# Performance work log

Measured on AMD Instinct MI355X. Metric: run time of the kernel, lower is better.

## Reference

```python
import jax, jax.numpy as jnp
import numpy as np

D_MODEL = 1024
N_HEADS = 16
HEAD_DIM = D_MODEL // N_HEADS


def setup_inputs() -> dict:
    key = jax.random.key(0)
    ks = jax.random.split(key, 5)
    B, T = 2, 2048
    x = jax.random.normal(ks[0], (B, T, D_MODEL), dtype=jnp.float32)
    s_in = 1.0 / np.sqrt(D_MODEL)
    W_qkv = jax.random.normal(ks[1], (D_MODEL, 3 * D_MODEL), dtype=jnp.float32) * s_in
    b_qkv = jnp.zeros((3 * D_MODEL,), dtype=jnp.float32)
    W_out = jax.random.normal(ks[2], (D_MODEL, D_MODEL), dtype=jnp.float32) * s_in
    b_out = jnp.zeros((D_MODEL,), dtype=jnp.float32)
    gamma = jnp.ones((D_MODEL,), dtype=jnp.float32)
    beta = jnp.zeros((D_MODEL,), dtype=jnp.float32)
    return {"x": x, "W_qkv": W_qkv, "b_qkv": b_qkv, "W_out": W_out,
            "b_out": b_out, "gamma": gamma, "beta": beta}


def _layernorm(x, gamma, beta, eps=1e-5):
    mu = jnp.mean(x, axis=-1, keepdims=True)
    var = jnp.var(x, axis=-1, keepdims=True)
    return (x - mu) * jax.lax.rsqrt(var + eps) * gamma + beta


def reference(x, W_qkv, b_qkv, W_out, b_out, gamma, beta):
    B, T, D = x.shape
    residual = x
    h = _layernorm(x, gamma, beta)
    qkv = h @ W_qkv + b_qkv                      # [B, T, 3D]
    qkv = qkv.reshape(B, T, 3, N_HEADS, HEAD_DIM)
    q = jnp.transpose(qkv[:, :, 0], (0, 2, 1, 3))  # [B, H, T, hd]
    k = jnp.transpose(qkv[:, :, 1], (0, 2, 1, 3))
    v = jnp.transpose(qkv[:, :, 2], (0, 2, 1, 3))
    scale = 1.0 / np.sqrt(HEAD_DIM)
    attn = jnp.einsum("bhqd,bhkd->bhqk", q, k) * scale
    attn = jax.nn.softmax(attn, axis=-1)
    out = jnp.einsum("bhqk,bhkd->bhqd", attn, v)   # [B, H, T, hd]
    out = jnp.transpose(out, (0, 2, 1, 3)).reshape(B, T, D)
    out = out @ W_out + b_out
    return residual + out
```

## Files before the change

kernel.cpp:

```cpp
#include <hip/hip_runtime.h>
#include <hip/hip_bf16.h>


#define DINL static __device__ __forceinline__

typedef __attribute__((ext_vector_type(8))) short bf16x8;
typedef __attribute__((ext_vector_type(4))) float f32x4;

DINL float fast_exp2(float x) { return __builtin_amdgcn_exp2f(x); }

DINL unsigned short f2bf(float f) {
  __hip_bfloat16 h = __float2bfloat16(f);
  unsigned short u;
  __builtin_memcpy(&u, &h, 2);
  return u;
}

DINL unsigned int bfbits(float f) {
  unsigned int u;
  __builtin_memcpy(&u, &f, 4);
  return (u + 0x8000u) >> 16;
}

DINL void gload_lds16(const void* g, void* l) {
  __builtin_amdgcn_global_load_lds((__attribute__((address_space(1))) void*)g,
                                   (__attribute__((address_space(3))) void*)l,
                                   16, 0, 0);
}

__global__ __launch_bounds__(256)
void ln_kernel(const float* __restrict__ x, const float* __restrict__ gamma,
               const float* __restrict__ beta, unsigned short* __restrict__ h) {
  __shared__ float red[8];
  int row = blockIdx.x;
  int t = threadIdx.x;
  float4 v = reinterpret_cast<const float4*>(x + (size_t)row * 1024)[t];
  float s  = v.x + v.y + v.z + v.w;
  float sq = v.x*v.x + v.y*v.y + v.z*v.z + v.w*v.w;
#pragma unroll
  for (int off = 1; off < 64; off <<= 1) {
    s  += __shfl_xor(s, off);
    sq += __shfl_xor(sq, off);
  }
  int wid = t >> 6;
  if ((t & 63) == 0) { red[wid] = s; red[4 + wid] = sq; }
  __syncthreads();
  s  = red[0] + red[1] + red[2] + red[3];
  sq = red[4] + red[5] + red[6] + red[7];
  float mu   = s * (1.0f / 1024.0f);
  float var  = sq * (1.0f / 1024.0f) - mu * mu;
  float rstd = rsqrtf(var + 1e-5f);
  float4 g = reinterpret_cast<const float4*>(gamma)[t];
  float4 b = reinterpret_cast<const float4*>(beta)[t];
  ushort4 o;
  o.x = f2bf((v.x - mu) * rstd * g.x + b.x);
  o.y = f2bf((v.y - mu) * rstd * g.y + b.y);
  o.z = f2bf((v.z - mu) * rstd * g.z + b.z);
  o.w = f2bf((v.w - mu) * rstd * g.w + b.w);
  reinterpret_cast<ushort4*>(h + (size_t)row * 1024)[t] = o;
}

__global__ __launch_bounds__(256)
void transpose_cast_kernel(const float* __restrict__ src, unsigned short* __restrict__ dst,
                           int R, int C) {
  __shared__ float tile[32][33];
  int tx = threadIdx.x & 31, ty = threadIdx.x >> 5;
  int c0 = blockIdx.x * 32, r0 = blockIdx.y * 32;
#pragma unroll
  for (int i = 0; i < 4; i++)
    tile[ty + i * 8][tx] = src[(size_t)(r0 + ty + i * 8) * C + c0 + tx];
  __syncthreads();
#pragma unroll
  for (int i = 0; i < 4; i++) {
    int r = ty + i * 8;
    dst[(size_t)(c0 + r) * R + r0 + tx] = f2bf(tile[tx][r]);
  }
}

template <int MODE>
__global__ __launch_bounds__(256)
void gemm128(const unsigned short* __restrict__ A,
             const unsigned short* __restrict__ Bt,
             int K,
             const float* __restrict__ bias,
             unsigned short* __restrict__ qdst, unsigned short* __restrict__ kdst,
             unsigned short* __restrict__ vTdst,
             const float* __restrict__ xres, float* __restrict__ out) {
  __shared__ unsigned short As[8192];
  __shared__ unsigned short Bs[8192];
  int tid = threadIdx.x, wid = tid >> 6, lane = tid & 63;
  int l15 = lane & 15, l4 = lane >> 4;
  int brow = blockIdx.y * 128, bcol = blockIdx.x * 128;
  int wr = wid >> 1, wc = wid & 1;
  f32x4 acc[4][4] = {};

  for (int kt = 0; kt < K; kt += 64) {
    __syncthreads();
#pragma unroll
    for (int r = 0; r < 4; r++) {
      int c  = wid * 256 + r * 64;
      int cl = c + lane;
      int kb = cl >> 7, row = cl & 127;
      gload_lds16(A  + (size_t)(brow + row) * K + kt + kb * 8, As + c * 8);
      gload_lds16(Bt + (size_t)(bcol + row) * K + kt + kb * 8, Bs + c * 8);
    }
    __syncthreads();
#pragma unroll
    for (int ks = 0; ks < 2; ks++) {
      int kb = ks * 4 + l4;
      bf16x8 af[4], bfr[4];
#pragma unroll
      for (int m = 0; m < 4; m++)
        af[m] = *reinterpret_cast<const bf16x8*>(As + (kb * 128 + wr * 64 + m * 16 + l15) * 8);
#pragma unroll
      for (int n = 0; n < 4; n++)
        bfr[n] = *reinterpret_cast<const bf16x8*>(Bs + (kb * 128 + wc * 64 + n * 16 + l15) * 8);
#pragma unroll
      for (int m = 0; m < 4; m++)
#pragma unroll
        for (int n = 0; n < 4; n++)
          acc[m][n] = __builtin_amdgcn_mfma_f32_16x16x32_bf16(af[m], bfr[n], acc[m][n], 0, 0, 0);
    }
  }

  if (MODE == 0) {
    int sec = bcol >> 10;
    int secbase = sec << 10;
#pragma unroll
    for (int m = 0; m < 4; m++) {
      int row0 = brow + wr * 64 + m * 16 + l4 * 4;
      int b = row0 >> 11, t0 = row0 & 2047;
#pragma unroll
      for (int n = 0; n < 4; n++) {
        int col = (bcol & 1023) + wc * 64 + n * 16 + l15;
        float bv = bias[secbase + col];
        int hh = col >> 6, d = col & 63;
        if (sec == 2) {
          ushort4 pk;
          pk.x = f2bf(acc[m][n][0] + bv);
          pk.y = f2bf(acc[m][n][1] + bv);
          pk.z = f2bf(acc[m][n][2] + bv);
          pk.w = f2bf(acc[m][n][3] + bv);
          *reinterpret_cast<ushort4*>(vTdst + ((size_t)(b * 16 + hh) * 64 + d) * 2048 + t0) = pk;
        } else {
          unsigned short* dst = (sec == 0) ? qdst : kdst;
          float sc = (sec == 0) ? 0.125f * 1.44269504088896f : 1.0f;
#pragma unroll
          for (int j = 0; j < 4; j++)
            dst[((size_t)(b * 16 + hh) * 2048 + t0 + j) * 64 + d] = f2bf((acc[m][n][j] + bv) * sc);
        }
      }
    }
  } else {
#pragma unroll
    for (int m = 0; m < 4; m++) {
      int row0 = brow + wr * 64 + m * 16 + l4 * 4;
#pragma unroll
      for (int n = 0; n < 4; n++) {
        int col = bcol + wc * 64 + n * 16 + l15;
        float bv = bias[col];
#pragma unroll
        for (int j = 0; j < 4; j++) {
          size_t idx = (size_t)(row0 + j) * 1024 + col;
          out[idx] = acc[m][n][j] + bv + xres[idx];
        }
      }
    }
  }
}

__global__ __launch_bounds__(256, 2)
void attn_kernel(const unsigned short* __restrict__ q,
                 const unsigned short* __restrict__ kk,
                 const unsigned short* __restrict__ vT,
                 unsigned short* __restrict__ o) {
  const int T = 2048;
  __shared__ unsigned short Ks[2][8192];
  __shared__ unsigned short Ps[4][2048];
  int tid = threadIdx.x, wid = tid >> 6, lane = tid & 63;
  int l15 = lane & 15, l4 = lane >> 4;
  int swz = (l15 & 7) << 3;

  int lin = blockIdx.x;
  int rl  = (lin & 7) * 64 + (lin >> 3);
  int bx = rl & 15, bh = rl >> 4;
  int q0 = bx * 128 + wid * 32;

  const unsigned short* qh = q  + (size_t)bh * T * 64;
  const unsigned short* kh = kk + (size_t)bh * T * 64;
  const unsigned short* vh = vT + (size_t)bh * 64 * T;

  bf16x8 qf[2][2];
#pragma unroll
  for (int m = 0; m < 2; m++)
#pragma unroll
    for (int ks = 0; ks < 2; ks++)
      qf[m][ks] = *reinterpret_cast<const bf16x8*>(
          qh + (size_t)(q0 + m * 16 + l15) * 64 + ks * 32 + l4 * 8);

  f32x4 accO[2][4] = {};
  float mst[2] = {-1e30f, -1e30f}, lst[2] = {0.0f, 0.0f};

#define STAGE128(buf, kv0)                                                     \
  {                                                                            \
    _Pragma("unroll") for (int r = 0; r < 4; r++) {                            \
      int c  = (wid * 4 + r) * 64;                                             \
      int cl = c + lane;                                                       \
      int key = cl >> 3;                                                       \
      int kb  = (cl & 7) ^ (key & 7);                                          \
      gload_lds16(kh + (size_t)((kv0) + key) * 64 + kb * 8, &Ks[buf][c * 8]);  \
    }                                                                          \
  }

#define SUBTILE(sub, vf)                                                       \
  {                                                                            \
    f32x4 s[2][4] = {};                                                        \
    __builtin_amdgcn_s_setprio(1);                                             \
    _Pragma("unroll") for (int ks = 0; ks < 2; ks++) {                         \
      _Pragma("unroll") for (int n = 0; n < 4; n++) {                          \
        int kkey = (sub) * 64 + n * 16 + l15;                                  \
        int slot = kkey * 8 + ((ks * 4 + l4) ^ (kkey & 7));                    \
        bf16x8 kf = *reinterpret_cast<const bf16x8*>(&Ks[cur][slot * 8]);      \
        _Pragma("unroll") for (int m = 0; m < 2; m++)                          \
          s[m][n] = __builtin_amdgcn_mfma_f32_16x16x32_bf16(kf, qf[m][ks],     \
                                                            s[m][n], 0, 0, 0); \
      }                                                                        \
    }                                                                          \
    __builtin_amdgcn_s_setprio(0);                                             \
    float mx[2];                                                               \
    _Pragma("unroll") for (int m = 0; m < 2; m++) {                            \
      float a0 = fmaxf(fmaxf(s[m][0][0], s[m][0][1]),                          \
                       fmaxf(s[m][0][2], s[m][0][3]));                         \
      float a1 = fmaxf(fmaxf(s[m][1][0], s[m][1][1]),                          \
                       fmaxf(s[m][1][2], s[m][1][3]));                         \
      float a2 = fmaxf(fmaxf(s[m][2][0], s[m][2][1]),                          \
                       fmaxf(s[m][2][2], s[m][2][3]));                         \
      float a3 = fmaxf(fmaxf(s[m][3][0], s[m][3][1]),                          \
                       fmaxf(s[m][3][2], s[m][3][3]));                         \
      float mxv = fmaxf(fmaxf(a0, a1), fmaxf(a2, a3));                         \
      mxv = fmaxf(mxv, __shfl_xor(mxv, 16));                                   \
      mxv = fmaxf(mxv, __shfl_xor(mxv, 32));                                   \
      mx[m] = mxv;                                                             \
    }                                                                          \
    int defer = (mx[0] <= mst[0] + 11.0f) && (mx[1] <= mst[1] + 11.0f);        \
    if (__all(defer)) {                                                        \
      _Pragma("unroll") for (int m = 0; m < 2; m++) {                          \
        float sum = 0.0f;                                                      \
        _Pragma("unroll") for (int n = 0; n < 4; n++) {                        \
          _Pragma("unroll") for (int j = 0; j < 4; j++) {                      \
            float p = fast_exp2(s[m][n][j] - mst[m]);                          \
            s[m][n][j] = p;                                                    \
            sum += p;                                                          \
          }                                                                    \
          unsigned int u0 = bfbits(s[m][n][0]) | (bfbits(s[m][n][1]) << 16);   \
          unsigned int u1 = bfbits(s[m][n][2]) | (bfbits(s[m][n][3]) << 16);   \
          *reinterpret_cast<uint2*>(                                           \
              &Ps[wid][(m * 16 + l15) * 64 + ((n * 16 + l4 * 4) ^ swz)]) =     \
              make_uint2(u0, u1);                                              \
        }                                                                      \
        lst[m] += sum;                                                         \
      }                                                                        \
    } else {                                                                   \
      _Pragma("unroll") for (int m = 0; m < 2; m++) {                          \
        float mnew = fmaxf(mst[m], mx[m]);                                     \
        float a = fast_exp2(mst[m] - mnew);                                    \
        float sum = 0.0f;                                                      \
        _Pragma("unroll") for (int n = 0; n < 4; n++) {                        \
          _Pragma("unroll") for (int j = 0; j < 4; j++) {                      \
            float p = fast_exp2(s[m][n][j] - mnew);                            \
            s[m][n][j] = p;                                                    \
            sum += p;                                                          \
          }                                                                    \
          unsigned int u0 = bfbits(s[m][n][0]) | (bfbits(s[m][n][1]) << 16);   \
          unsigned int u1 = bfbits(s[m][n][2]) | (bfbits(s[m][n][3]) << 16);   \
          *reinterpret_cast<uint2*>(                                           \
              &Ps[wid][(m * 16 + l15) * 64 + ((n * 16 + l4 * 4) ^ swz)]) =     \
              make_uint2(u0, u1);                                              \
        }                                                                      \
        lst[m] = lst[m] * a + sum;                                             \
        mst[m] = mnew;                                                         \
        _Pragma("unroll") for (int n = 0; n < 4; n++)                          \
          _Pragma("unroll") for (int j = 0; j < 4; j++) accO[m][n][j] *= a;    \
      }                                                                        \
    }                                                                          \
    _Pragma("unroll") for (int ks = 0; ks < 2; ks++) {                         \
      _Pragma("unroll") for (int m = 0; m < 2; m++) {                          \
        bf16x8 pf = *reinterpret_cast<const bf16x8*>(                          \
            &Ps[wid][(m * 16 + l15) * 64 + ((ks * 32 + l4 * 8) ^ swz)]);       \
        __builtin_amdgcn_s_setprio(1);                                         \
        _Pragma("unroll") for (int n = 0; n < 4; n++)                          \
          accO[m][n] = __builtin_amdgcn_mfma_f32_16x16x32_bf16(                \
              vf[ks][n], pf, accO[m][n], 0, 0, 0);                             \
        __builtin_amdgcn_s_setprio(0);                                         \
      }                                                                        \
    }                                                                          \
  }

#define LOADV(vf, kvs)                                                         \
  {                                                                            \
    _Pragma("unroll") for (int ks = 0; ks < 2; ks++)                           \
      _Pragma("unroll") for (int n = 0; n < 4; n++)                            \
        vf[ks][n] = *reinterpret_cast<const bf16x8*>(                          \
            vh + (size_t)(n * 16 + l15) * T + (kvs) + ks * 32 + l4 * 8);       \
  }

  STAGE128(0, 0);
  __syncthreads();
  int cur = 0;

  for (int kv0 = 0; kv0 < T; kv0 += 128) {
    bf16x8 vf0[2][4];
    LOADV(vf0, kv0);
    if (kv0 + 128 < T) STAGE128(cur ^ 1, kv0 + 128);
    SUBTILE(0, vf0);
    bf16x8 vf1[2][4];
    LOADV(vf1, kv0 + 64);
    SUBTILE(1, vf1);
    __syncthreads();
    cur ^= 1;
  }
#undef SUBTILE
#undef LOADV
#undef STAGE128

  int b = bh >> 4, hh = bh & 15;
#pragma unroll
  for (int m = 0; m < 2; m++) {
    float l = lst[m];
    l += __shfl_xor(l, 16);
    l += __shfl_xor(l, 32);
    float inv = 1.0f / l;
    int row = q0 + m * 16 + l15;
#pragma unroll
    for (int n = 0; n < 4; n++) {
      ushort4 pk;
      pk.x = f2bf(accO[m][n][0] * inv);
      pk.y = f2bf(accO[m][n][1] * inv);
      pk.z = f2bf(accO[m][n][2] * inv);
      pk.w = f2bf(accO[m][n][3] * inv);
      *reinterpret_cast<ushort4*>(
          &o[(size_t)(b * 2048 + row) * 1024 + hh * 64 + n * 16 + l4 * 4]) = pk;
    }
  }
}

extern "C" void kernel_launch(void* const* d_in, const int* in_sizes, int n_in,
                              void* d_out, int out_size, void* d_ws, size_t ws_size,
                              hipStream_t stream) {
  const float* x     = (const float*)d_in[0];
  const float* W_qkv = (const float*)d_in[1];
  const float* b_qkv = (const float*)d_in[2];
  const float* W_out = (const float*)d_in[3];
  const float* b_out = (const float*)d_in[4];
  const float* gamma = (const float*)d_in[5];
  const float* beta  = (const float*)d_in[6];
  float* out = (float*)d_out;

  char* ws = (char*)d_ws;
  unsigned short* h     = (unsigned short*)(ws);
  unsigned short* WqkvT = (unsigned short*)(ws + (size_t)(8)  * 1024 * 1024);
  unsigned short* WoutT = (unsigned short*)(ws + (size_t)(14) * 1024 * 1024);
  unsigned short* qb    = (unsigned short*)(ws + (size_t)(16) * 1024 * 1024);
  unsigned short* kb    = (unsigned short*)(ws + (size_t)(24) * 1024 * 1024);
  unsigned short* vTb   = (unsigned short*)(ws + (size_t)(32) * 1024 * 1024);
  unsigned short* attno = (unsigned short*)(ws + (size_t)(40) * 1024 * 1024);

  ln_kernel<<<4096, 256, 0, stream>>>(x, gamma, beta, h);
  transpose_cast_kernel<<<dim3(96, 32), 256, 0, stream>>>(W_qkv, WqkvT, 1024, 3072);
  transpose_cast_kernel<<<dim3(32, 32), 256, 0, stream>>>(W_out, WoutT, 1024, 1024);
  gemm128<0><<<dim3(24, 32), 256, 0, stream>>>(h, WqkvT, 1024, b_qkv, qb, kb, vTb, nullptr, nullptr);
  attn_kernel<<<512, 256, 0, stream>>>(qb, kb, vTb, attno);
  gemm128<1><<<dim3(8, 32), 256, 0, stream>>>(attno, WoutT, 1024, b_out, nullptr, nullptr, nullptr, x, out);
}
```

Measured before the change: 183.2 us.

## Halve attention and output-GEMM tile heights to launch more blocks

The attention kernel now gives each wave 16 query rows instead of 32, with 64 queries per block, so it launches 1024 blocks and raises the occupancy hint to 4. The output projection GEMM gets a templated BM=64 row tile, doubling its grid from 256 to 512 blocks. The goal is to fill all CUs on the device and improve latency hiding. The cost is more K/V staging traffic per query and less MFMA reuse of each loaded K/V fragment.

```diff
diff --git a/kernel.cpp b/kernel.cpp
--- a/kernel.cpp
+++ b/kernel.cpp
@@ -77,7 +77,7 @@
   }
 }
 
-template <int MODE>
+template <int BM, int MODE>
 __global__ __launch_bounds__(256)
 void gemm128(const unsigned short* __restrict__ A,
              const unsigned short* __restrict__ Bt,
@@ -86,37 +86,45 @@
              unsigned short* __restrict__ qdst, unsigned short* __restrict__ kdst,
              unsigned short* __restrict__ vTdst,
              const float* __restrict__ xres, float* __restrict__ out) {
-  __shared__ unsigned short As[8192];
+  static_assert(BM == 128 || BM == 64, "");
+  constexpr int MR = BM / 32;
+  __shared__ unsigned short As[BM * 64];
   __shared__ unsigned short Bs[8192];
   int tid = threadIdx.x, wid = tid >> 6, lane = tid & 63;
   int l15 = lane & 15, l4 = lane >> 4;
-  int brow = blockIdx.y * 128, bcol = blockIdx.x * 128;
+  int brow = blockIdx.y * BM, bcol = blockIdx.x * 128;
   int wr = wid >> 1, wc = wid & 1;
-  f32x4 acc[4][4] = {};
+  f32x4 acc[MR][4] = {};
 
   for (int kt = 0; kt < K; kt += 64) {
     __syncthreads();
+#pragma unroll
+    for (int r = 0; r < MR; r++) {
+      int c  = wid * (BM * 2) + r * 64;
+      int cl = c + lane;
+      int kb = cl / BM, row = cl % BM;
+      gload_lds16(A + (size_t)(brow + row) * K + kt + kb * 8, As + c * 8);
+    }
 #pragma unroll
     for (int r = 0; r < 4; r++) {
       int c  = wid * 256 + r * 64;
       int cl = c + lane;
       int kb = cl >> 7, row = cl & 127;
-      gload_lds16(A  + (size_t)(brow + row) * K + kt + kb * 8, As + c * 8);
       gload_lds16(Bt + (size_t)(bcol + row) * K + kt + kb * 8, Bs + c * 8);
     }
     __syncthreads();
 #pragma unroll
     for (int ks = 0; ks < 2; ks++) {
       int kb = ks * 4 + l4;
-      bf16x8 af[4], bfr[4];
-#pragma unroll
-      for (int m = 0; m < 4; m++)
-        af[m] = *reinterpret_cast<const bf16x8*>(As + (kb * 128 + wr * 64 + m * 16 + l15) * 8);
+      bf16x8 af[MR], bfr[4];
+#pragma unroll
+      for (int m = 0; m < MR; m++)
+        af[m] = *reinterpret_cast<const bf16x8*>(As + (kb * BM + wr * (BM / 2) + m * 16 + l15) * 8);
 #pragma unroll
       for (int n = 0; n < 4; n++)
         bfr[n] = *reinterpret_cast<const bf16x8*>(Bs + (kb * 128 + wc * 64 + n * 16 + l15) * 8);
 #pragma unroll
-      for (int m = 0; m < 4; m++)
+      for (int m = 0; m < MR; m++)
 #pragma unroll
         for (int n = 0; n < 4; n++)
           acc[m][n] = __builtin_amdgcn_mfma_f32_16x16x32_bf16(af[m], bfr[n], acc[m][n], 0, 0, 0);
@@ -127,8 +135,8 @@
     int sec = bcol >> 10;
     int secbase = sec << 10;
 #pragma unroll
-    for (int m = 0; m < 4; m++) {
-      int row0 = brow + wr * 64 + m * 16 + l4 * 4;
+    for (int m = 0; m < MR; m++) {
+      int row0 = brow + wr * (BM / 2) + m * 16 + l4 * 4;
       int b = row0 >> 11, t0 = row0 & 2047;
 #pragma unroll
       for (int n = 0; n < 4; n++) {
@@ -153,8 +161,8 @@
     }
   } else {
 #pragma unroll
-    for (int m = 0; m < 4; m++) {
-      int row0 = brow + wr * 64 + m * 16 + l4 * 4;
+    for (int m = 0; m < MR; m++) {
+      int row0 = brow + wr * (BM / 2) + m * 16 + l4 * 4;
 #pragma unroll
       for (int n = 0; n < 4; n++) {
         int col = bcol + wc * 64 + n * 16 + l15;
@@ -169,37 +177,35 @@
   }
 }
 
-__global__ __launch_bounds__(256, 2)
+__global__ __launch_bounds__(256, 4)
 void attn_kernel(const unsigned short* __restrict__ q,
                  const unsigned short* __restrict__ kk,
                  const unsigned short* __restrict__ vT,
                  unsigned short* __restrict__ o) {
   const int T = 2048;
   __shared__ unsigned short Ks[2][8192];
-  __shared__ unsigned short Ps[4][2048];
+  __shared__ unsigned short Ps[4][1024];
   int tid = threadIdx.x, wid = tid >> 6, lane = tid & 63;
   int l15 = lane & 15, l4 = lane >> 4;
   int swz = (l15 & 7) << 3;
 
   int lin = blockIdx.x;
-  int rl  = (lin & 7) * 64 + (lin >> 3);
-  int bx = rl & 15, bh = rl >> 4;
-  int q0 = bx * 128 + wid * 32;
+  int rl  = (lin & 7) * 128 + (lin >> 3);
+  int bx = rl & 31, bh = rl >> 5;
+  int q0 = bx * 64 + wid * 16;
 
   const unsigned short* qh = q  + (size_t)bh * T * 64;
   const unsigned short* kh = kk + (size_t)bh * T * 64;
   const unsigned short* vh = vT + (size_t)bh * 64 * T;
 
-  bf16x8 qf[2][2];
-#pragma unroll
-  for (int m = 0; m < 2; m++)
-#pragma unroll
-    for (int ks = 0; ks < 2; ks++)
-      qf[m][ks] = *reinterpret_cast<const bf16x8*>(
-          qh + (size_t)(q0 + m * 16 + l15) * 64 + ks * 32 + l4 * 8);
-
-  f32x4 accO[2][4] = {};
-  float mst[2] = {-1e30f, -1e30f}, lst[2] = {0.0f, 0.0f};
+  bf16x8 qf[2];
+#pragma unroll
+  for (int ks = 0; ks < 2; ks++)
+    qf[ks] = *reinterpret_cast<const bf16x8*>(
+        qh + (size_t)(q0 + l15) * 64 + ks * 32 + l4 * 8);
+
+  f32x4 accO[4] = {};
+  float mst = -1e30f, lst = 0.0f;
 
 #define STAGE128(buf, kv0)                                                     \
   {                                                                            \
@@ -214,85 +220,69 @@
 
 #define SUBTILE(sub, vf)                                                       \
   {                                                                            \
-    f32x4 s[2][4] = {};                                                        \
+    f32x4 s[4] = {};                                                           \
     __builtin_amdgcn_s_setprio(1);                                             \
     _Pragma("unroll") for (int ks = 0; ks < 2; ks++) {                         \
       _Pragma("unroll") for (int n = 0; n < 4; n++) {                          \
         int kkey = (sub) * 64 + n * 16 + l15;                                  \
         int slot = kkey * 8 + ((ks * 4 + l4) ^ (kkey & 7));                    \
         bf16x8 kf = *reinterpret_cast<const bf16x8*>(&Ks[cur][slot * 8]);      \
-        _Pragma("unroll") for (int m = 0; m < 2; m++)                          \
-          s[m][n] = __builtin_amdgcn_mfma_f32_16x16x32_bf16(kf, qf[m][ks],     \
-                                                            s[m][n], 0, 0, 0); \
+        s[n] = __builtin_amdgcn_mfma_f32_16x16x32_bf16(kf, qf[ks],             \
+                                                       s[n], 0, 0, 0);         \
       }                                                                        \
     }                                                                          \
     __builtin_amdgcn_s_setprio(0);                                             \
-    float mx[2];                                                               \
-    _Pragma("unroll") for (int m = 0; m < 2; m++) {                            \
-      float a0 = fmaxf(fmaxf(s[m][0][0], s[m][0][1]),                          \
-                       fmaxf(s[m][0][2], s[m][0][3]));                         \
-      float a1 = fmaxf(fmaxf(s[m][1][0], s[m][1][1]),                          \
-                       fmaxf(s[m][1][2], s[m][1][3]));                         \
-      float a2 = fmaxf(fmaxf(s[m][2][0], s[m][2][1]),                          \
-                       fmaxf(s[m][2][2], s[m][2][3]));                         \
-      float a3 = fmaxf(fmaxf(s[m][3][0], s[m][3][1]),                          \
-                       fmaxf(s[m][3][2], s[m][3][3]));                         \
-      float mxv = fmaxf(fmaxf(a0, a1), fmaxf(a2, a3));                         \
-      mxv = fmaxf(mxv, __shfl_xor(mxv, 16));                                   \
-      mxv = fmaxf(mxv, __shfl_xor(mxv, 32));                                   \
-      mx[m] = mxv;                                                             \
-    }                                                                          \
-    int defer = (mx[0] <= mst[0] + 11.0f) && (mx[1] <= mst[1] + 11.0f);        \
-    if (__all(defer)) {                                                        \
-      _Pragma("unroll") for (int m = 0; m < 2; m++) {                          \
-        float sum = 0.0f;                                                      \
-        _Pragma("unroll") for (int n = 0; n < 4; n++) {                        \
-          _Pragma("unroll") for (int j = 0; j < 4; j++) {                      \
-            float p = fast_exp2(s[m][n][j] - mst[m]);                          \
-            s[m][n][j] = p;                                                    \
-            sum += p;                                                          \
-          }                                                                    \
-          unsigned int u0 = bfbits(s[m][n][0]) | (bfbits(s[m][n][1]) << 16);   \
-          unsigned int u1 = bfbits(s[m][n][2]) | (bfbits(s[m][n][3]) << 16);   \
-          *reinterpret_cast<uint2*>(                                           \
-              &Ps[wid][(m * 16 + l15) * 64 + ((n * 16 + l4 * 4) ^ swz)]) =     \
-              make_uint2(u0, u1);                                              \
+    float a0 = fmaxf(fmaxf(s[0][0], s[0][1]), fmaxf(s[0][2], s[0][3]));        \
+    float a1 = fmaxf(fmaxf(s[1][0], s[1][1]), fmaxf(s[1][2], s[1][3]));        \
+    float a2 = fmaxf(fmaxf(s[2][0], s[2][1]), fmaxf(s[2][2], s[2][3]));        \
+    float a3 = fmaxf(fmaxf(s[3][0], s[3][1]), fmaxf(s[3][2], s[3][3]));        \
+    float mx = fmaxf(fmaxf(a0, a1), fmaxf(a2, a3));                            \
+    mx = fmaxf(mx, __shfl_xor(mx, 16));                                        \
+    mx = fmaxf(mx, __shfl_xor(mx, 32));                                        \
+    if (__all(mx <= mst + 11.0f)) {                                            \
+      float sum = 0.0f;                                                        \
+      _Pragma("unroll") for (int n = 0; n < 4; n++) {                          \
+        _Pragma("unroll") for (int j = 0; j < 4; j++) {                        \
+          float p = fast_exp2(s[n][j] - mst);                                  \
+          s[n][j] = p;                                                         \
+          sum += p;                                                            \
         }                                                                      \
-        lst[m] += sum;                                                         \
+        unsigned int u0 = bfbits(s[n][0]) | (bfbits(s[n][1]) << 16);           \
+        unsigned int u1 = bfbits(s[n][2]) | (bfbits(s[n][3]) << 16);           \
+        *reinterpret_cast<uint2*>(                                             \
+            &Ps[wid][l15 * 64 + ((n * 16 + l4 * 4) ^ swz)]) =                  \
+            make_uint2(u0, u1);                                                \
       }                                                                        \
+      lst += sum;                                                              \
     } else {                                                                   \
-      _Pragma("unroll") for (int m = 0; m < 2; m++) {                          \
-        float mnew = fmaxf(mst[m], mx[m]);                                     \
-        float a = fast_exp2(mst[m] - mnew);                                    \
-        float sum = 0.0f;                                                      \
-        _Pragma("unroll") for (int n = 0; n < 4; n++) {                        \
-          _Pragma("unroll") for (int j = 0; j < 4; j++) {                      \
-            float p = fast_exp2(s[m][n][j] - mnew);                            \
-            s[m][n][j] = p;                                                    \
-            sum += p;                                                          \
-          }                                                                    \
-          unsigned int u0 = bfbits(s[m][n][0]) | (bfbits(s[m][n][1]) << 16);   \
-          unsigned int u1 = bfbits(s[m][n][2]) | (bfbits(s[m][n][3]) << 16);   \
-          *reinterpret_cast<uint2*>(                                           \
-              &Ps[wid][(m * 16 + l15) * 64 + ((n * 16 + l4 * 4) ^ swz)]) =     \
-              make_uint2(u0, u1);                                              \
+      float mnew = fmaxf(mst, mx);                                             \
+      float a = fast_exp2(mst - mnew);                                         \
+      float sum = 0.0f;                                                        \
+      _Pragma("unroll") for (int n = 0; n < 4; n++) {                          \
+        _Pragma("unroll") for (int j = 0; j < 4; j++) {                        \
+          float p = fast_exp2(s[n][j] - mnew);                                 \
+          s[n][j] = p;                                                         \
+          sum += p;                                                            \
         }                                                                      \
-        lst[m] = lst[m] * a + sum;                                             \
-        mst[m] = mnew;                                                         \
-        _Pragma("unroll") for (int n = 0; n < 4; n++)                          \
-          _Pragma("unroll") for (int j = 0; j < 4; j++) accO[m][n][j] *= a;    \
+        unsigned int u0 = bfbits(s[n][0]) | (bfbits(s[n][1]) << 16);           \
+        unsigned int u1 = bfbits(s[n][2]) | (bfbits(s[n][3]) << 16);           \
+        *reinterpret_cast<uint2*>(                                             \
+            &Ps[wid][l15 * 64 + ((n * 16 + l4 * 4) ^ swz)]) =                  \
+            make_uint2(u0, u1);                                                \
       }                                                                        \
+      lst = lst * a + sum;                                                     \
+      mst = mnew;                                                              \
+      _Pragma("unroll") for (int n = 0; n < 4; n++)                            \
+        _Pragma("unroll") for (int j = 0; j < 4; j++) accO[n][j] *= a;         \
     }                                                                          \
     _Pragma("unroll") for (int ks = 0; ks < 2; ks++) {                         \
-      _Pragma("unroll") for (int m = 0; m < 2; m++) {                          \
-        bf16x8 pf = *reinterpret_cast<const bf16x8*>(                          \
-            &Ps[wid][(m * 16 + l15) * 64 + ((ks * 32 + l4 * 8) ^ swz)]);       \
-        __builtin_amdgcn_s_setprio(1);                                         \
-        _Pragma("unroll") for (int n = 0; n < 4; n++)                          \
-          accO[m][n] = __builtin_amdgcn_mfma_f32_16x16x32_bf16(                \
-              vf[ks][n], pf, accO[m][n], 0, 0, 0);                             \
-        __builtin_amdgcn_s_setprio(0);                                         \
-      }                                                                        \
+      bf16x8 pf = *reinterpret_cast<const bf16x8*>(                            \
+          &Ps[wid][l15 * 64 + ((ks * 32 + l4 * 8) ^ swz)]);                    \
+      __builtin_amdgcn_s_setprio(1);                                           \
+      _Pragma("unroll") for (int n = 0; n < 4; n++)                            \
+        accO[n] = __builtin_amdgcn_mfma_f32_16x16x32_bf16(                     \
+            vf[ks][n], pf, accO[n], 0, 0, 0);                                  \
+      __builtin_amdgcn_s_setprio(0);                                           \
     }                                                                          \
   }
 
@@ -324,23 +314,20 @@
 #undef STAGE128
 
   int b = bh >> 4, hh = bh & 15;
-#pragma unroll
-  for (int m = 0; m < 2; m++) {
-    float l = lst[m];
-    l += __shfl_xor(l, 16);
-    l += __shfl_xor(l, 32);
-    float inv = 1.0f / l;
-    int row = q0 + m * 16 + l15;
-#pragma unroll
-    for (int n = 0; n < 4; n++) {
-      ushort4 pk;
-      pk.x = f2bf(accO[m][n][0] * inv);
-      pk.y = f2bf(accO[m][n][1] * inv);
-      pk.z = f2bf(accO[m][n][2] * inv);
-      pk.w = f2bf(accO[m][n][3] * inv);
-      *reinterpret_cast<ushort4*>(
-          &o[(size_t)(b * 2048 + row) * 1024 + hh * 64 + n * 16 + l4 * 4]) = pk;
-    }
+  float l = lst;
+  l += __shfl_xor(l, 16);
+  l += __shfl_xor(l, 32);
+  float inv = 1.0f / l;
+  int row = q0 + l15;
+#pragma unroll
+  for (int n = 0; n < 4; n++) {
+    ushort4 pk;
+    pk.x = f2bf(accO[n][0] * inv);
+    pk.y = f2bf(accO[n][1] * inv);
+    pk.z = f2bf(accO[n][2] * inv);
+    pk.w = f2bf(accO[n][3] * inv);
+    *reinterpret_cast<ushort4*>(
+        &o[(size_t)(b * 2048 + row) * 1024 + hh * 64 + n * 16 + l4 * 4]) = pk;
   }
 }
 
@@ -368,7 +355,7 @@
   ln_kernel<<<4096, 256, 0, stream>>>(x, gamma, beta, h);
   transpose_cast_kernel<<<dim3(96, 32), 256, 0, stream>>>(W_qkv, WqkvT, 1024, 3072);
   transpose_cast_kernel<<<dim3(32, 32), 256, 0, stream>>>(W_out, WoutT, 1024, 1024);
-  gemm128<0><<<dim3(24, 32), 256, 0, stream>>>(h, WqkvT, 1024, b_qkv, qb, kb, vTb, nullptr, nullptr);
-  attn_kernel<<<512, 256, 0, stream>>>(qb, kb, vTb, attno);
-  gemm128<1><<<dim3(8, 32), 256, 0, stream>>>(attno, WoutT, 1024, b_out, nullptr, nullptr, nullptr, x, out);
-}
+  gemm128<128, 0><<<dim3(24, 32), 256, 0, stream>>>(h, WqkvT, 1024, b_qkv, qb, kb, vTb, nullptr, nullptr);
+  attn_kernel<<<1024, 256, 0, stream>>>(qb, kb, vTb, attno);
+  gemm128<64, 1><<<dim3(8, 64), 256, 0, stream>>>(attno, WoutT, 1024, b_out, nullptr, nullptr, nullptr, x, out);
+}
```

Result: slower. 233.3 us (+27.3%).
